# Optimization experiments

Hardware: AMD Instinct MI355X
Metric: run time of the kernel (lower is better)

Reference implementation:

```python
import jax, jax.numpy as jnp
import numpy as np

BLOCKSIZE = 128
KEEPER = 128


def setup_inputs() -> dict:
    key = jax.random.key(0)
    ks = jax.random.split(key, 8)
    S, H = 2048, 4096
    n_nonout = H - KEEPER          # 3968
    nb = n_nonout // BLOCKSIZE     # 31 low-precision blocks
    return {
        "x": jax.random.normal(ks[0], (1, S, H), dtype=jnp.float32),
        "weight": jax.random.normal(ks[1], (H, H), dtype=jnp.float32),   # [out, in]
        "scales": jax.random.uniform(ks[2], (H, n_nonout), dtype=jnp.float32),
        "keep_scales": jax.random.uniform(ks[3], (H, 1), dtype=jnp.float32),
        "inp_scales_lo": jax.random.uniform(ks[4], (S, nb), dtype=jnp.float32),
        "inp_scales_hi": jax.random.uniform(ks[5], (S, 1), dtype=jnp.float32),
        "inp_base_lo": jax.random.uniform(ks[6], (S, nb), dtype=jnp.float32),
        "inp_base_hi": jax.random.uniform(ks[7], (S, 1), dtype=jnp.float32),
    }


def reference(x, weight, scales, keep_scales, inp_scales_lo, inp_scales_hi,
              inp_base_lo, inp_base_hi):
    # Faithful vectorization of QLinearLayer._forward (channel_group == 0, bias None).
    bs, S, H = x.shape
    xs = x[0]                      # [S, H]  (bs == 1 assert in original)
    W = weight.T                   # [H, O]
    n_nonout = H - KEEPER
    nb = n_nonout // BLOCKSIZE
    O = W.shape[1]

    # Per-block weight scales: scales[:, i1] for each block start i1 -> [nb, O]
    w_blk_scales = scales[:, 0:n_nonout:BLOCKSIZE].T              # [nb, O]

    # Blockwise outer-product scaling fused into the operands:
    # y[s,o] = sum_n sc_lo[s,n] * ws[n,o] * (x_block_n @ W_block_n)[s,o]
    x_lo = xs[:, :n_nonout].reshape(S, nb, BLOCKSIZE) * inp_scales_lo[:, :, None]
    W_lo = W[:n_nonout, :].reshape(nb, BLOCKSIZE, O) * w_blk_scales[:, None, :]
    y = x_lo.reshape(S, n_nonout) @ W_lo.reshape(n_nonout, O)     # [S, O]

    # int8 keeper channels (high-precision path)
    hi_scales = inp_scales_hi @ keep_scales.T                      # [S, O]
    y_hi = xs[:, n_nonout:] @ W[n_nonout:, :]                      # [S, O]
    y = y + y_hi * hi_scales

    return y.reshape(bs, S, O)
```

## Files before the change

### kernel.cpp

```cpp
#include <hip/hip_runtime.h>

#define S_DIM 2048
#define K_DIM 4096
#define O_DIM 4096
#define NNON  3968
#define NB    31

typedef __bf16 bf16x8 __attribute__((ext_vector_type(8)));
typedef float  f32x4  __attribute__((ext_vector_type(4)));

__device__ __forceinline__ unsigned short f2bf(float f) {
    union { float f; unsigned u; } v; v.f = f;
    unsigned r = v.u + 0x7FFFu + ((v.u >> 16) & 1u);
    return (unsigned short)(r >> 16);
}

__global__ __launch_bounds__(256) void scale_x(const float* __restrict__ x,
                                               const float* __restrict__ sc_lo,
                                               const float* __restrict__ sc_hi,
                                               unsigned short* __restrict__ A)
{
    int idx = blockIdx.x * 256 + threadIdx.x;
    int s = idx >> 10;
    int k = (idx & 1023) << 2;
    float4 v = ((const float4*)x)[idx];
    float sc = (k < NNON) ? sc_lo[s * NB + (k >> 7)] : sc_hi[s];
    ushort4 o;
    o.x = f2bf(v.x * sc); o.y = f2bf(v.y * sc);
    o.z = f2bf(v.z * sc); o.w = f2bf(v.w * sc);
    ((ushort4*)A)[idx] = o;
}

__global__ __launch_bounds__(256) void scale_w(const float* __restrict__ w,
                                               const float* __restrict__ scales,
                                               const float* __restrict__ keep,
                                               unsigned short* __restrict__ B)
{
    int idx = blockIdx.x * 256 + threadIdx.x;
    int o = idx >> 10;
    int k = (idx & 1023) << 2;
    float4 v = ((const float4*)w)[idx];
    float sc = (k < NNON) ? scales[(size_t)o * NNON + ((k >> 7) << 7)] : keep[o];
    ushort4 r;
    r.x = f2bf(v.x * sc); r.y = f2bf(v.y * sc);
    r.z = f2bf(v.z * sc); r.w = f2bf(v.w * sc);
    ((ushort4*)B)[idx] = r;
}

#define BM 128
#define BN 128
#define BK 64

__global__ __launch_bounds__(256) void gemm_bt(const unsigned short* __restrict__ A,
                                               const unsigned short* __restrict__ B,
                                               float* __restrict__ C)
{
    __shared__ unsigned short As[BM * BK];
    __shared__ unsigned short Bs[BN * BK];

    const int tid  = threadIdx.x;
    const int wave = tid >> 6;
    const int lane = tid & 63;
    const int quad = lane >> 4;
    const int l16  = lane & 15;
    const int bm = blockIdx.y * BM;
    const int bn = blockIdx.x * BN;
    const int wm = (wave >> 1) * 64;
    const int wn = (wave & 1) * 64;

    const int srow = (lane >> 3);
    const int scol = (((lane & 7) ^ (srow & 7)) << 3);
    const int swz  = (l16 & 7);

    f32x4 acc[4][4];
    #pragma unroll
    for (int i = 0; i < 4; ++i)
        #pragma unroll
        for (int j = 0; j < 4; ++j)
            acc[i][j] = (f32x4){0.f, 0.f, 0.f, 0.f};

    for (int k0 = 0; k0 < K_DIM; k0 += BK) {
        __syncthreads();
        #pragma unroll
        for (int c = 0; c < 4; ++c) {
            const int row = wave * 32 + c * 8 + srow;
            __builtin_amdgcn_global_load_lds(
                (__attribute__((address_space(1))) unsigned int*)(A + (size_t)(bm + row) * K_DIM + k0 + scol),
                (__attribute__((address_space(3))) unsigned int*)(&As[(wave * 4 + c) * 512]),
                16, 0, 0);
            __builtin_amdgcn_global_load_lds(
                (__attribute__((address_space(1))) unsigned int*)(B + (size_t)(bn + row) * K_DIM + k0 + scol),
                (__attribute__((address_space(3))) unsigned int*)(&Bs[(wave * 4 + c) * 512]),
                16, 0, 0);
        }
        __syncthreads();

        #pragma unroll
        for (int ks = 0; ks < 2; ++ks) {
            bf16x8 af[4], bfr[4];
            #pragma unroll
            for (int i = 0; i < 4; ++i)
                af[i] = *(const bf16x8*)(&As[(wm + i * 16 + l16) * BK + (((ks * 4 + quad) ^ swz) << 3)]);
            #pragma unroll
            for (int j = 0; j < 4; ++j)
                bfr[j] = *(const bf16x8*)(&Bs[(wn + j * 16 + l16) * BK + (((ks * 4 + quad) ^ swz) << 3)]);
            #pragma unroll
            for (int i = 0; i < 4; ++i)
                #pragma unroll
                for (int j = 0; j < 4; ++j)
                    acc[i][j] = __builtin_amdgcn_mfma_f32_16x16x32_bf16(af[i], bfr[j], acc[i][j], 0, 0, 0);
        }
    }

    #pragma unroll
    for (int i = 0; i < 4; ++i)
        #pragma unroll
        for (int j = 0; j < 4; ++j) {
            const int col = bn + wn + j * 16 + l16;
            #pragma unroll
            for (int r = 0; r < 4; ++r) {
                const int row = bm + wm + i * 16 + quad * 4 + r;
                C[(size_t)row * O_DIM + col] = acc[i][j][r];
            }
        }
}

extern "C" void kernel_launch(void* const* d_in, const int* in_sizes, int n_in,
                              void* d_out, int out_size, void* d_ws, size_t ws_size,
                              hipStream_t stream) {
    const float* x      = (const float*)d_in[0];
    const float* weight = (const float*)d_in[1];
    const float* scales = (const float*)d_in[2];
    const float* keep   = (const float*)d_in[3];
    const float* sc_lo  = (const float*)d_in[4];
    const float* sc_hi  = (const float*)d_in[5];

    unsigned short* A = (unsigned short*)d_ws;
    unsigned short* B = A + (size_t)S_DIM * K_DIM;

    scale_x<<<(S_DIM * K_DIM / 4) / 256, 256, 0, stream>>>(x, sc_lo, sc_hi, A);
    scale_w<<<(O_DIM * K_DIM / 4) / 256, 256, 0, stream>>>(weight, scales, keep, B);

    dim3 grid(O_DIM / BN, S_DIM / BM);
    gemm_bt<<<grid, 256, 0, stream>>>(A, B, (float*)d_out);
}
```

Baseline: 259.6 us.

## Split GEMM K dimension in two with atomic accumulation and merge prepass kernels

The bf16 GEMM now splits K into two halves across a third grid dimension and accumulates partial results into the output with float atomic adds. The output is zeroed in a combined prepass kernel that also does the x and weight scaling, replacing two launches with one. The aim is to raise the block count from 512 to 1024 so the many compute units stay busy, at the cost of an extra output zeroing pass and atomic write traffic.

```diff
diff --git a/kernel.cpp b/kernel.cpp
--- a/kernel.cpp
+++ b/kernel.cpp
@@ -5,6 +5,10 @@
 #define O_DIM 4096
 #define NNON  3968
 #define NB    31
+
+#define XBLK 8192
+#define WBLK 16384
+#define ZBLK 8192
 
 typedef __bf16 bf16x8 __attribute__((ext_vector_type(8)));
 typedef float  f32x4  __attribute__((ext_vector_type(4)));
@@ -15,41 +19,48 @@
     return (unsigned short)(r >> 16);
 }
 
-__global__ __launch_bounds__(256) void scale_x(const float* __restrict__ x,
+__global__ __launch_bounds__(256) void prepass(const float* __restrict__ x,
                                                const float* __restrict__ sc_lo,
                                                const float* __restrict__ sc_hi,
-                                               unsigned short* __restrict__ A)
-{
-    int idx = blockIdx.x * 256 + threadIdx.x;
-    int s = idx >> 10;
-    int k = (idx & 1023) << 2;
-    float4 v = ((const float4*)x)[idx];
-    float sc = (k < NNON) ? sc_lo[s * NB + (k >> 7)] : sc_hi[s];
-    ushort4 o;
-    o.x = f2bf(v.x * sc); o.y = f2bf(v.y * sc);
-    o.z = f2bf(v.z * sc); o.w = f2bf(v.w * sc);
-    ((ushort4*)A)[idx] = o;
-}
-
-__global__ __launch_bounds__(256) void scale_w(const float* __restrict__ w,
+                                               const float* __restrict__ w,
                                                const float* __restrict__ scales,
                                                const float* __restrict__ keep,
-                                               unsigned short* __restrict__ B)
+                                               unsigned short* __restrict__ A,
+                                               unsigned short* __restrict__ B,
+                                               float* __restrict__ C)
 {
-    int idx = blockIdx.x * 256 + threadIdx.x;
-    int o = idx >> 10;
-    int k = (idx & 1023) << 2;
-    float4 v = ((const float4*)w)[idx];
-    float sc = (k < NNON) ? scales[(size_t)o * NNON + ((k >> 7) << 7)] : keep[o];
-    ushort4 r;
-    r.x = f2bf(v.x * sc); r.y = f2bf(v.y * sc);
-    r.z = f2bf(v.z * sc); r.w = f2bf(v.w * sc);
-    ((ushort4*)B)[idx] = r;
+    const int b = blockIdx.x;
+    if (b < XBLK) {
+        int idx = b * 256 + threadIdx.x;
+        int s = idx >> 10;
+        int k = (idx & 1023) << 2;
+        float4 v = ((const float4*)x)[idx];
+        float sc = (k < NNON) ? sc_lo[s * NB + (k >> 7)] : sc_hi[s];
+        ushort4 o;
+        o.x = f2bf(v.x * sc); o.y = f2bf(v.y * sc);
+        o.z = f2bf(v.z * sc); o.w = f2bf(v.w * sc);
+        ((ushort4*)A)[idx] = o;
+    } else if (b < XBLK + WBLK) {
+        int idx = (b - XBLK) * 256 + threadIdx.x;
+        int o = idx >> 10;
+        int k = (idx & 1023) << 2;
+        float4 v = ((const float4*)w)[idx];
+        float sc = (k < NNON) ? scales[(size_t)o * NNON + ((k >> 7) << 7)] : keep[o];
+        ushort4 r;
+        r.x = f2bf(v.x * sc); r.y = f2bf(v.y * sc);
+        r.z = f2bf(v.z * sc); r.w = f2bf(v.w * sc);
+        ((ushort4*)B)[idx] = r;
+    } else {
+        int idx = (b - XBLK - WBLK) * 256 + threadIdx.x;
+        ((float4*)C)[idx] = make_float4(0.f, 0.f, 0.f, 0.f);
+    }
 }
 
 #define BM 128
 #define BN 128
 #define BK 64
+#define KSPLIT 2
+#define KHALF (K_DIM / KSPLIT)
 
 __global__ __launch_bounds__(256) void gemm_bt(const unsigned short* __restrict__ A,
                                                const unsigned short* __restrict__ B,
@@ -65,6 +76,7 @@
     const int l16  = lane & 15;
     const int bm = blockIdx.y * BM;
     const int bn = blockIdx.x * BN;
+    const int kz = blockIdx.z;
     const int wm = (wave >> 1) * 64;
     const int wn = (wave & 1) * 64;
 
@@ -79,7 +91,8 @@
         for (int j = 0; j < 4; ++j)
             acc[i][j] = (f32x4){0.f, 0.f, 0.f, 0.f};
 
-    for (int k0 = 0; k0 < K_DIM; k0 += BK) {
+    const int kbeg = kz * KHALF;
+    for (int k0 = kbeg; k0 < kbeg + KHALF; k0 += BK) {
         __syncthreads();
         #pragma unroll
         for (int c = 0; c < 4; ++c) {
@@ -120,7 +133,7 @@
             #pragma unroll
             for (int r = 0; r < 4; ++r) {
                 const int row = bm + wm + i * 16 + quad * 4 + r;
-                C[(size_t)row * O_DIM + col] = acc[i][j][r];
+                unsafeAtomicAdd(&C[(size_t)row * O_DIM + col], acc[i][j][r]);
             }
         }
 }
@@ -137,10 +150,10 @@
 
     unsigned short* A = (unsigned short*)d_ws;
     unsigned short* B = A + (size_t)S_DIM * K_DIM;
+    float* C = (float*)d_out;
 
-    scale_x<<<(S_DIM * K_DIM / 4) / 256, 256, 0, stream>>>(x, sc_lo, sc_hi, A);
-    scale_w<<<(O_DIM * K_DIM / 4) / 256, 256, 0, stream>>>(weight, scales, keep, B);
+    prepass<<<XBLK + WBLK + ZBLK, 256, 0, stream>>>(x, sc_lo, sc_hi, weight, scales, keep, A, B, C);
 
-    dim3 grid(O_DIM / BN, S_DIM / BM);
-    gemm_bt<<<grid, 256, 0, stream>>>(A, B, (float*)d_out);
+    dim3 grid(O_DIM / BN, S_DIM / BM, KSPLIT);
+    gemm_bt<<<grid, 256, 0, stream>>>(A, B, C);
 }
```

Measured after the change: 295.1 us. +13.7%, slower.

## Merge scaling prepasses into one launch and prefetch next GEMM tile into LDS

Applied to the files above, without the earlier changes.

The two bf16 scaling kernels become one launch that dispatches on block index, removing a kernel launch and its tail. In the GEMM, the LDS fragments for the whole K-step are loaded into registers first, then the next tile's global-to-LDS loads are issued before the MFMAs, so global latency overlaps with compute. This raises register pressure (doubled fragment arrays) and keeps two barriers per iteration.

```diff
diff --git a/kernel.cpp b/kernel.cpp
--- a/kernel.cpp
+++ b/kernel.cpp
@@ -5,6 +5,9 @@
 #define O_DIM 4096
 #define NNON  3968
 #define NB    31
+
+#define XBLK 8192
+#define WBLK 16384
 
 typedef __bf16 bf16x8 __attribute__((ext_vector_type(8)));
 typedef float  f32x4  __attribute__((ext_vector_type(4)));
@@ -15,36 +18,37 @@
     return (unsigned short)(r >> 16);
 }
 
-__global__ __launch_bounds__(256) void scale_x(const float* __restrict__ x,
+__global__ __launch_bounds__(256) void prepass(const float* __restrict__ x,
                                                const float* __restrict__ sc_lo,
                                                const float* __restrict__ sc_hi,
-                                               unsigned short* __restrict__ A)
-{
-    int idx = blockIdx.x * 256 + threadIdx.x;
-    int s = idx >> 10;
-    int k = (idx & 1023) << 2;
-    float4 v = ((const float4*)x)[idx];
-    float sc = (k < NNON) ? sc_lo[s * NB + (k >> 7)] : sc_hi[s];
-    ushort4 o;
-    o.x = f2bf(v.x * sc); o.y = f2bf(v.y * sc);
-    o.z = f2bf(v.z * sc); o.w = f2bf(v.w * sc);
-    ((ushort4*)A)[idx] = o;
-}
-
-__global__ __launch_bounds__(256) void scale_w(const float* __restrict__ w,
+                                               const float* __restrict__ w,
                                                const float* __restrict__ scales,
                                                const float* __restrict__ keep,
+                                               unsigned short* __restrict__ A,
                                                unsigned short* __restrict__ B)
 {
-    int idx = blockIdx.x * 256 + threadIdx.x;
-    int o = idx >> 10;
-    int k = (idx & 1023) << 2;
-    float4 v = ((const float4*)w)[idx];
-    float sc = (k < NNON) ? scales[(size_t)o * NNON + ((k >> 7) << 7)] : keep[o];
-    ushort4 r;
-    r.x = f2bf(v.x * sc); r.y = f2bf(v.y * sc);
-    r.z = f2bf(v.z * sc); r.w = f2bf(v.w * sc);
-    ((ushort4*)B)[idx] = r;
+    const int b = blockIdx.x;
+    if (b < XBLK) {
+        int idx = b * 256 + threadIdx.x;
+        int s = idx >> 10;
+        int k = (idx & 1023) << 2;
+        float4 v = ((const float4*)x)[idx];
+        float sc = (k < NNON) ? sc_lo[s * NB + (k >> 7)] : sc_hi[s];
+        ushort4 o;
+        o.x = f2bf(v.x * sc); o.y = f2bf(v.y * sc);
+        o.z = f2bf(v.z * sc); o.w = f2bf(v.w * sc);
+        ((ushort4*)A)[idx] = o;
+    } else {
+        int idx = (b - XBLK) * 256 + threadIdx.x;
+        int o = idx >> 10;
+        int k = (idx & 1023) << 2;
+        float4 v = ((const float4*)w)[idx];
+        float sc = (k < NNON) ? scales[(size_t)o * NNON + ((k >> 7) << 7)] : keep[o];
+        ushort4 r;
+        r.x = f2bf(v.x * sc); r.y = f2bf(v.y * sc);
+        r.z = f2bf(v.z * sc); r.w = f2bf(v.w * sc);
+        ((ushort4*)B)[idx] = r;
+    }
 }
 
 #define BM 128
@@ -72,6 +76,9 @@
     const int scol = (((lane & 7) ^ (srow & 7)) << 3);
     const int swz  = (l16 & 7);
 
+    const unsigned short* Abase = A + (size_t)(bm + wave * 32 + srow) * K_DIM + scol;
+    const unsigned short* Bbase = B + (size_t)(bn + wave * 32 + srow) * K_DIM + scol;
+
     f32x4 acc[4][4];
     #pragma unroll
     for (int i = 0; i < 4; ++i)
@@ -79,37 +86,56 @@
         for (int j = 0; j < 4; ++j)
             acc[i][j] = (f32x4){0.f, 0.f, 0.f, 0.f};
 
+    #pragma unroll
+    for (int c = 0; c < 4; ++c) {
+        __builtin_amdgcn_global_load_lds(
+            (__attribute__((address_space(1))) unsigned int*)(Abase + (size_t)(c * 8) * K_DIM),
+            (__attribute__((address_space(3))) unsigned int*)(&As[(wave * 4 + c) * 512]),
+            16, 0, 0);
+        __builtin_amdgcn_global_load_lds(
+            (__attribute__((address_space(1))) unsigned int*)(Bbase + (size_t)(c * 8) * K_DIM),
+            (__attribute__((address_space(3))) unsigned int*)(&Bs[(wave * 4 + c) * 512]),
+            16, 0, 0);
+    }
+    __syncthreads();
+
     for (int k0 = 0; k0 < K_DIM; k0 += BK) {
-        __syncthreads();
+        bf16x8 af[2][4], bfr[2][4];
         #pragma unroll
-        for (int c = 0; c < 4; ++c) {
-            const int row = wave * 32 + c * 8 + srow;
-            __builtin_amdgcn_global_load_lds(
-                (__attribute__((address_space(1))) unsigned int*)(A + (size_t)(bm + row) * K_DIM + k0 + scol),
-                (__attribute__((address_space(3))) unsigned int*)(&As[(wave * 4 + c) * 512]),
-                16, 0, 0);
-            __builtin_amdgcn_global_load_lds(
-                (__attribute__((address_space(1))) unsigned int*)(B + (size_t)(bn + row) * K_DIM + k0 + scol),
-                (__attribute__((address_space(3))) unsigned int*)(&Bs[(wave * 4 + c) * 512]),
-                16, 0, 0);
+        for (int ks = 0; ks < 2; ++ks) {
+            #pragma unroll
+            for (int i = 0; i < 4; ++i)
+                af[ks][i] = *(const bf16x8*)(&As[(wm + i * 16 + l16) * BK + (((ks * 4 + quad) ^ swz) << 3)]);
+            #pragma unroll
+            for (int j = 0; j < 4; ++j)
+                bfr[ks][j] = *(const bf16x8*)(&Bs[(wn + j * 16 + l16) * BK + (((ks * 4 + quad) ^ swz) << 3)]);
         }
         __syncthreads();
 
+        if (k0 + BK < K_DIM) {
+            const size_t koff = (size_t)(k0 + BK);
+            #pragma unroll
+            for (int c = 0; c < 4; ++c) {
+                __builtin_amdgcn_global_load_lds(
+                    (__attribute__((address_space(1))) unsigned int*)(Abase + (size_t)(c * 8) * K_DIM + koff),
+                    (__attribute__((address_space(3))) unsigned int*)(&As[(wave * 4 + c) * 512]),
+                    16, 0, 0);
+                __builtin_amdgcn_global_load_lds(
+                    (__attribute__((address_space(1))) unsigned int*)(Bbase + (size_t)(c * 8) * K_DIM + koff),
+                    (__attribute__((address_space(3))) unsigned int*)(&Bs[(wave * 4 + c) * 512]),
+                    16, 0, 0);
+            }
+        }
+
         #pragma unroll
-        for (int ks = 0; ks < 2; ++ks) {
-            bf16x8 af[4], bfr[4];
-            #pragma unroll
-            for (int i = 0; i < 4; ++i)
-                af[i] = *(const bf16x8*)(&As[(wm + i * 16 + l16) * BK + (((ks * 4 + quad) ^ swz) << 3)]);
-            #pragma unroll
-            for (int j = 0; j < 4; ++j)
-                bfr[j] = *(const bf16x8*)(&Bs[(wn + j * 16 + l16) * BK + (((ks * 4 + quad) ^ swz) << 3)]);
+        for (int ks = 0; ks < 2; ++ks)
             #pragma unroll
             for (int i = 0; i < 4; ++i)
                 #pragma unroll
                 for (int j = 0; j < 4; ++j)
-                    acc[i][j] = __builtin_amdgcn_mfma_f32_16x16x32_bf16(af[i], bfr[j], acc[i][j], 0, 0, 0);
-        }
+                    acc[i][j] = __builtin_amdgcn_mfma_f32_16x16x32_bf16(af[ks][i], bfr[ks][j], acc[i][j], 0, 0, 0);
+
+        __syncthreads();
     }
 
     #pragma unroll
@@ -138,8 +164,7 @@
     unsigned short* A = (unsigned short*)d_ws;
     unsigned short* B = A + (size_t)S_DIM * K_DIM;
 
-    scale_x<<<(S_DIM * K_DIM / 4) / 256, 256, 0, stream>>>(x, sc_lo, sc_hi, A);
-    scale_w<<<(O_DIM * K_DIM / 4) / 256, 256, 0, stream>>>(weight, scales, keep, B);
+    prepass<<<XBLK + WBLK, 256, 0, stream>>>(x, sc_lo, sc_hi, weight, scales, keep, A, B);
 
     dim3 grid(O_DIM / BN, S_DIM / BM);
     gemm_bt<<<grid, 256, 0, stream>>>(A, B, (float*)d_out);
```

Result: faster. 246.8 us (-4.9%).
